# Optimization experiments

Measured on AMD Instinct MI355X. Metric: run time of the kernel, lower is better.

Reference implementation:

```python
import jax, jax.numpy as jnp
import numpy as np

EMB = 2048
HEADS = 16
HEAD_DIM = EMB // HEADS
MIN_WINDOW = 64
MAX_WINDOW = 256
ROPE_BASE = 10000.0


def setup_inputs() -> dict:
    key = jax.random.key(0)
    ks = jax.random.split(key, 5)
    B, S = 2, 2048
    x = jax.random.normal(ks[0], (B, S, EMB), dtype=jnp.float32)
    w_qkv = jax.random.normal(ks[1], (3 * EMB, EMB), dtype=jnp.float32) * (EMB ** -0.5)
    w_out = jax.random.normal(ks[2], (EMB, EMB), dtype=jnp.float32) * (EMB ** -0.5)
    w_c1 = jax.random.normal(ks[3], (EMB // 4, EMB), dtype=jnp.float32) * 0.1 * (EMB ** -0.5)
    w_c2 = jax.random.normal(ks[4], (1, EMB // 4), dtype=jnp.float32) * 0.1 * ((EMB // 4) ** -0.5)
    return {"x": x, "w_qkv": w_qkv, "w_out": w_out, "w_c1": w_c1, "w_c2": w_c2}


def _rotate_half(t):
    # interleaved pairs: [-x1, x0, -x3, x2, ...]
    x1 = t[..., ::2]
    x2 = t[..., 1::2]
    return jnp.stack((-x2, x1), axis=-1).reshape(t.shape)


def _rope_tables(seq_len, dtype):
    inv_freq = 1.0 / (ROPE_BASE ** (jnp.arange(0, HEAD_DIM, 2, dtype=jnp.float32) / HEAD_DIM))
    pos = jnp.arange(seq_len, dtype=jnp.float32)
    freqs = jnp.outer(pos, inv_freq)                      # [S, D/2]
    emb = jnp.concatenate([freqs, freqs], axis=-1)        # [S, D]
    return jnp.cos(emb)[None, None].astype(dtype), jnp.sin(emb)[None, None].astype(dtype)


def _forward(x, w_qkv, w_out, w_c1, w_c2):
    B, S, _ = x.shape
    scale = HEAD_DIM ** -0.5

    qkv = x @ w_qkv.T                                     # [B, S, 3E]
    qkv = qkv.reshape(B, S, 3, HEADS, HEAD_DIM).transpose(2, 0, 3, 1, 4)
    q, k, v = qkv[0], qkv[1], qkv[2]                      # each [B, H, S, D]

    cos, sin = _rope_tables(S, x.dtype)
    q = q * cos + _rotate_half(q) * sin
    k = k * cos + _rotate_half(k) * sin

    scores = jnp.einsum("bhqd,bhkd->bhqk", q, k) * scale  # [B, H, S, S]

    # adaptive window size from input complexity
    var = jnp.var(x.reshape(B, -1), axis=1, ddof=1)        # torch unbiased var over dims [1,2]
    var_norm = jax.nn.sigmoid(var * 10.0 - 5.0)
    x_mean = x.mean(axis=1)                                # [B, E]
    hidden = jax.nn.silu(x_mean @ w_c1.T)
    learned = jax.nn.sigmoid(hidden @ w_c2.T)[:, 0]        # [B]
    complexity = (var_norm + learned) / 2.0
    window_f = MIN_WINDOW + complexity * (MAX_WINDOW - MIN_WINDOW)
    window = window_f.mean().astype(jnp.int32)             # trunc like .int()
    window = jnp.maximum(jnp.minimum(window, S), MIN_WINDOW)

    # causal + sliding-window mask: keep 0 <= q_pos - k_pos < window
    pos = jnp.arange(S)
    rel = pos[:, None] - pos[None, :]                      # [S, S]
    keep = (rel >= 0) & (rel < window)
    scores = jnp.where(keep[None, None], scores, -jnp.inf)

    attn = jax.nn.softmax(scores, axis=-1)
    out = jnp.einsum("bhqk,bhkd->bhqd", attn, v)           # [B, H, S, D]
    out = out.transpose(0, 2, 1, 3).reshape(B, S, EMB)
    return out @ w_out.T


def reference(x, w_qkv, w_out, w_c1, w_c2):
    return _forward(x, w_qkv, w_out, w_c1, w_c2)
```

## Files before the change

### kernel.cpp

```cpp
#include <hip/hip_runtime.h>
#include <math.h>


#define S_LEN 2048
#define EMB 2048
#define HEADS 16
#define HDIM 128
#define NT 20
#define PSTR 336

typedef _Float16 f16x8 __attribute__((ext_vector_type(8)));
typedef _Float16 f16x4 __attribute__((ext_vector_type(4)));
typedef float f32x4 __attribute__((ext_vector_type(4)));

__device__ __forceinline__ void gld16(const void* g, void* l) {
    __builtin_amdgcn_global_load_lds(
        (const __attribute__((address_space(1))) unsigned int*)g,
        (__attribute__((address_space(3))) unsigned int*)l, 16, 0, 0);
}

__global__ void rope_table(float2* __restrict__ cstab) {
    int s = blockIdx.x;
    int d = threadIdx.x;
    int j = d & 63;
    double inv = pow(10000.0, -(double)j / 64.0);
    double ang = (double)s * inv;
    cstab[s * HDIM + d] = make_float2((float)cos(ang), (float)sin(ang));
}

__global__ __launch_bounds__(256) void col_reduce(const float* __restrict__ x,
                                                  float* __restrict__ xmean_acc,
                                                  double* __restrict__ scal,
                                                  _Float16* __restrict__ x16) {
    int b = blockIdx.z;
    int cg = blockIdx.x;
    int sg = blockIdx.y;
    int e4 = cg * 256 + threadIdx.x;
    const size_t base = ((size_t)b * S_LEN + sg * 32) * EMB;
    const float4* xb = (const float4*)(x + base) + e4;
    f16x4* xo = (f16x4*)(x16 + base) + e4;
    double cs0 = 0.0, cs1 = 0.0, cs2 = 0.0, cs3 = 0.0;
    double cq = 0.0;
    for (int s = 0; s < 32; ++s) {
        float4 v = xb[(size_t)s * (EMB / 4)];
        f16x4 o;
        o.x = (_Float16)v.x; o.y = (_Float16)v.y;
        o.z = (_Float16)v.z; o.w = (_Float16)v.w;
        xo[(size_t)s * (EMB / 4)] = o;
        cs0 += v.x; cs1 += v.y; cs2 += v.z; cs3 += v.w;
        cq += (double)v.x * v.x + (double)v.y * v.y +
              (double)v.z * v.z + (double)v.w * v.w;
    }
    float* xm = xmean_acc + b * EMB + e4 * 4;
    atomicAdd(xm + 0, (float)cs0);
    atomicAdd(xm + 1, (float)cs1);
    atomicAdd(xm + 2, (float)cs2);
    atomicAdd(xm + 3, (float)cs3);
    __shared__ double rs[256], rq[256];
    rs[threadIdx.x] = cs0 + cs1 + cs2 + cs3;
    rq[threadIdx.x] = cq;
    __syncthreads();
    for (int off = 128; off > 0; off >>= 1) {
        if (threadIdx.x < off) {
            rs[threadIdx.x] += rs[threadIdx.x + off];
            rq[threadIdx.x] += rq[threadIdx.x + off];
        }
        __syncthreads();
    }
    if (threadIdx.x == 0) {
        atomicAdd(&scal[b], rs[0]);
        atomicAdd(&scal[2 + b], rq[0]);
    }
}

__global__ __launch_bounds__(256) void hidden_kernel(const float* __restrict__ xmean_acc,
                                                     const float* __restrict__ wc1,
                                                     float* __restrict__ hidden) {
    int j = blockIdx.x;
    int b = blockIdx.y;
    const float* xm = xmean_acc + b * EMB;
    const float* wr = wc1 + (size_t)j * EMB;
    double acc = 0.0;
    for (int k = threadIdx.x; k < EMB; k += 256)
        acc += (double)xm[k] * (double)wr[k];
    __shared__ double red[256];
    red[threadIdx.x] = acc;
    __syncthreads();
    for (int off = 128; off > 0; off >>= 1) {
        if (threadIdx.x < off) red[threadIdx.x] += red[threadIdx.x + off];
        __syncthreads();
    }
    if (threadIdx.x == 0) {
        double z = red[0] * (1.0 / 2048.0);
        hidden[b * 512 + j] = (float)(z / (1.0 + exp(-z)));
    }
}

__global__ __launch_bounds__(512) void window_kernel(const float* __restrict__ hidden,
                                                     const float* __restrict__ wc2,
                                                     const double* __restrict__ scal,
                                                     int* __restrict__ wout) {
    __shared__ double red[512];
    __shared__ double wfs[2];
    for (int b = 0; b < 2; ++b) {
        red[threadIdx.x] = (double)hidden[b * 512 + threadIdx.x] * (double)wc2[threadIdx.x];
        __syncthreads();
        for (int off = 256; off > 0; off >>= 1) {
            if (threadIdx.x < off) red[threadIdx.x] += red[threadIdx.x + off];
            __syncthreads();
        }
        if (threadIdx.x == 0) {
            double pre = red[0];
            double learned = 1.0 / (1.0 + exp(-pre));
            const double N = (double)S_LEN * (double)EMB;
            double sum = scal[b], sq = scal[2 + b];
            double var = (sq - sum * sum / N) / (N - 1.0);
            double vn = 1.0 / (1.0 + exp(-(var * 10.0 - 5.0)));
            double comp = 0.5 * (vn + learned);
            wfs[b] = 64.0 + comp * 192.0;
        }
        __syncthreads();
    }
    if (threadIdx.x == 0) {
        float wf = (float)(0.5 * (wfs[0] + wfs[1]));
        int w = (int)wf;
        if (w > S_LEN) w = S_LEN;
        if (w < 64) w = 64;
        *wout = w;
    }
}

#define NQKV4 3145728
#define NOUT4 1048576
__global__ __launch_bounds__(256) void cvt_weights(const float* __restrict__ wqkv,
                                                   const float* __restrict__ wout,
                                                   _Float16* __restrict__ d_qkv,
                                                   _Float16* __restrict__ d_out) {
    int i = blockIdx.x * 256 + threadIdx.x;
    const float4* s;
    f16x4* d;
    if (i < NQKV4) {
        s = (const float4*)wqkv + i;
        d = (f16x4*)d_qkv + i;
    } else {
        s = (const float4*)wout + (i - NQKV4);
        d = (f16x4*)d_out + (i - NQKV4);
    }
    float4 v = *s;
    f16x4 o;
    o.x = (_Float16)v.x; o.y = (_Float16)v.y;
    o.z = (_Float16)v.z; o.w = (_Float16)v.w;
    *d = o;
}

#define GEMM_PROLOGUE(An, Wn)                                                   \
    __shared__ _Float16 As[128 * 64];                                           \
    __shared__ _Float16 Bs[128 * 64];                                           \
    const int tid = threadIdx.x;                                                \
    const int lane = tid & 63;                                                  \
    const int wv = tid >> 6;                                                    \
    const int wm = wv >> 1, wn = wv & 1;                                        \
    const int m0 = blockIdx.y * 128;                                            \
    const int n0 = blockIdx.x * 128;                                            \
    const int lrow = lane >> 3;                                       \
    const int lchk = (lane & 7) ^ lrow;                       \
    const int srow = wv * 32 + lrow;                                            \
    const _Float16* agp = An + (size_t)(m0 + srow) * EMB + lchk * 8;            \
    const _Float16* bgp = Wn + (size_t)(n0 + srow) * EMB + lchk * 8;            \
    _Float16* al = &As[wv * 32 * 64];                                           \
    _Float16* bl = &Bs[wv * 32 * 64];                                           \
    const int frow = lane & 15;                                                 \
    const int fgrp = lane >> 4;                                                 \
    f32x4 acc[4][4] = {};                                                       \
    for (int k0 = 0; k0 < EMB; k0 += 64) {                                      \
        __syncthreads();                                                        \
        _Pragma("unroll")                                                       \
        for (int t = 0; t < 4; ++t) {                                           \
            gld16(agp + (size_t)t * 8 * EMB, al + t * 8 * 64);                  \
            gld16(bgp + (size_t)t * 8 * EMB, bl + t * 8 * 64);                  \
        }                                                                       \
        agp += 64; bgp += 64;                                                   \
        __syncthreads();                                                        \
        _Pragma("unroll")                                                       \
        for (int ks = 0; ks < 2; ++ks) {                                        \
            f16x8 af[4], bf[4];                                                 \
            _Pragma("unroll")                                                   \
            for (int i = 0; i < 4; ++i)                                         \
                af[i] = *(const f16x8*)&As[(wm * 64 + i * 16 + frow) * 64 +     \
                                           (((ks * 4 + fgrp) ^ (frow & 7)) * 8)]; \
            _Pragma("unroll")                                                   \
            for (int j = 0; j < 4; ++j)                                         \
                bf[j] = *(const f16x8*)&Bs[(wn * 64 + j * 16 + frow) * 64 +     \
                                           (((ks * 4 + fgrp) ^ (frow & 7)) * 8)]; \
            _Pragma("unroll")                                                   \
            for (int i = 0; i < 4; ++i)                                         \
                _Pragma("unroll")                                               \
                for (int j = 0; j < 4; ++j)                                     \
                    acc[i][j] = __builtin_amdgcn_mfma_f32_16x16x32_f16(         \
                        af[i], bf[j], acc[i][j], 0, 0, 0);                      \
        }                                                                       \
    }                                                                           \
    const int colbase = lane & 15;                                              \
    const int rowoff = (lane >> 4) * 4;

__global__ __launch_bounds__(256) void gemm_qkv_f16(const _Float16* __restrict__ An,
                                                    const _Float16* __restrict__ Wn,
                                                    _Float16* __restrict__ q16,
                                                    _Float16* __restrict__ k16,
                                                    _Float16* __restrict__ vt,
                                                    const float2* __restrict__ cstab) {
    GEMM_PROLOGUE(An, Wn)
    const int which = n0 >> 11;
    const int h = (n0 >> 7) & 15;
    if (which == 2) {
#pragma unroll
        for (int i = 0; i < 4; ++i) {
#pragma unroll
            for (int j = 0; j < 4; ++j) {
                const int d = wn * 64 + j * 16 + colbase;
                int m = m0 + wm * 64 + i * 16 + rowoff;
                int b = m >> 11, s = m & 2047;
                f16x4 o;
#pragma unroll
                for (int r = 0; r < 4; ++r) o[r] = (_Float16)acc[i][j][r];
                *(f16x4*)&vt[(((size_t)b * HEADS + h) * HDIM + d) * S_LEN + s] = o;
            }
        }
    } else {
        _Float16* dst = which == 0 ? q16 : k16;
        const float sgn = (colbase & 1) ? 1.f : -1.f;
#pragma unroll
        for (int i = 0; i < 4; ++i) {
#pragma unroll
            for (int j = 0; j < 4; ++j) {
                const int d = wn * 64 + j * 16 + colbase;
#pragma unroll
                for (int r = 0; r < 4; ++r) {
                    int m = m0 + wm * 64 + i * 16 + rowoff + r;
                    int b = m >> 11, s = m & 2047;
                    float a = acc[i][j][r];
                    float p = __shfl_xor(a, 1, 64);
                    float2 cs = cstab[(size_t)s * HDIM + d];
                    float o = fmaf(a, cs.x, sgn * p * cs.y);
                    dst[(((size_t)b * HEADS + h) * S_LEN + s) * HDIM + d] = (_Float16)o;
                }
            }
        }
    }
}

__global__ __launch_bounds__(256) void gemm_out_f16(const _Float16* __restrict__ An,
                                                    const _Float16* __restrict__ Wn,
                                                    float* __restrict__ C) {
    GEMM_PROLOGUE(An, Wn)
#pragma unroll
    for (int i = 0; i < 4; ++i) {
#pragma unroll
        for (int j = 0; j < 4; ++j) {
            const int n = n0 + wn * 64 + j * 16 + colbase;
#pragma unroll
            for (int r = 0; r < 4; ++r) {
                int m = m0 + wm * 64 + i * 16 + rowoff + r;
                C[(size_t)m * EMB + n] = acc[i][j][r];
            }
        }
    }
}

__global__ __launch_bounds__(256) void attn_mfma(const _Float16* __restrict__ q16,
                                                 const _Float16* __restrict__ k16,
                                                 const _Float16* __restrict__ v16t,
                                                 _Float16* __restrict__ ob,
                                                 const int* __restrict__ wptr) {
    const int q0 = blockIdx.x * 64;
    const int h = blockIdx.y;
    const int b = blockIdx.z;
    const int tid = threadIdx.x;
    const int lane = tid & 63;
    const int wv = tid >> 6;
    const int w = *wptr;

    __shared__ _Float16 Pl[4][16 * PSTR];
    _Float16* Pw = Pl[wv];

    const int kstart = q0 - 256;
    int ntlo_w = ((257 - w) >> 4) + wv;
    int ntlo_n = q0 < 256 ? ((256 - q0) >> 4) : 0;
    const int lo = ntlo_w > ntlo_n ? ntlo_w : ntlo_n;
    const int hi = wv + 17;
    const int pvlo = lo >> 1;
    const int pvhi = (hi + 1) >> 1;
    const int plo2 = pvlo << 1;
    const int phi2 = pvhi << 1;

    const int frow = lane & 15;
    const int fgrp = lane >> 4;
    const int fcol = fgrp * 8;

    const size_t bh = (size_t)b * HEADS + h;
    const _Float16* Qp = q16 + (bh * S_LEN + q0 + wv * 16 + frow) * HDIM + fcol;
    const _Float16* Kb = k16 + bh * S_LEN * HDIM;
    const _Float16* Vt = v16t + bh * HDIM * S_LEN;

    f16x8 aq[4];
#pragma unroll
    for (int ks = 0; ks < 4; ++ks) aq[ks] = *(const f16x8*)(Qp + ks * 32);

    f32x4 accs[NT];
#pragma unroll
    for (int nt = 0; nt < NT; ++nt) accs[nt] = (f32x4){0.f, 0.f, 0.f, 0.f};
#pragma unroll
    for (int nt = 0; nt < NT; ++nt) {
        if (nt < lo || nt >= hi) continue;
        int krow = kstart + nt * 16 + frow;
        if (krow < 0) krow = 0;
        const _Float16* kp = Kb + (size_t)krow * HDIM + fcol;
#pragma unroll
        for (int ks = 0; ks < 4; ++ks) {
            f16x8 bk = *(const f16x8*)(kp + ks * 32);
            accs[nt] = __builtin_amdgcn_mfma_f32_16x16x32_f16(aq[ks], bk, accs[nt], 0, 0, 0);
        }
    }

    const int qrow = fgrp * 4;
    const int qabs = q0 + wv * 16 + qrow;
    const float scale = 0.08838834764831845f;
    float mx[4] = {-INFINITY, -INFINITY, -INFINITY, -INFINITY};
#pragma unroll
    for (int nt = 0; nt < NT; ++nt) {
        if (nt < lo || nt >= hi) continue;
        int key = kstart + nt * 16 + frow;
#pragma unroll
        for (int r = 0; r < 4; ++r) {
            int rel = (qabs + r) - key;
            bool keep = (key >= 0) && (rel >= 0) && (rel < w);
            float s = keep ? accs[nt][r] * scale : -INFINITY;
            accs[nt][r] = s;
            mx[r] = fmaxf(mx[r], s);
        }
    }
#pragma unroll
    for (int r = 0; r < 4; ++r) {
        float m = mx[r];
#pragma unroll
        for (int off = 1; off < 16; off <<= 1)
            m = fmaxf(m, __shfl_xor(m, off, 64));
        mx[r] = m;
    }

    float ls[4] = {0.f, 0.f, 0.f, 0.f};
#pragma unroll
    for (int nt = 0; nt < NT; ++nt) {
        if (nt < plo2 || nt >= phi2) continue;
        const bool alive = (nt >= lo) && (nt < hi);
#pragma unroll
        for (int r = 0; r < 4; ++r) {
            float p = alive ? __expf(accs[nt][r] - mx[r]) : 0.f;
            ls[r] += p;
            Pw[(qrow + r) * PSTR + nt * 16 + frow] = (_Float16)p;
        }
    }
    float inv[4];
#pragma unroll
    for (int r = 0; r < 4; ++r) {
        float l = ls[r];
#pragma unroll
        for (int off = 1; off < 16; off <<= 1)
            l += __shfl_xor(l, off, 64);
        inv[r] = 1.f / l;
    }

    f32x4 acco[8];
#pragma unroll
    for (int jt = 0; jt < 8; ++jt) acco[jt] = (f32x4){0.f, 0.f, 0.f, 0.f};
    const _Float16* Pr = &Pl[wv][frow * PSTR];
#pragma unroll
    for (int kp = 0; kp < 10; ++kp) {
        if (kp < pvlo || kp >= pvhi) continue;
        f16x8 ap = *(const f16x8*)(Pr + kp * 32 + fcol);
        int kv = kstart + kp * 32 + fcol;
        if (kv < 0) kv = 0;
#pragma unroll
        for (int jt = 0; jt < 8; ++jt) {
            f16x8 bv = *(const f16x8*)(Vt + (size_t)(jt * 16 + frow) * S_LEN + kv);
            acco[jt] = __builtin_amdgcn_mfma_f32_16x16x32_f16(ap, bv, acco[jt], 0, 0, 0);
        }
    }

#pragma unroll
    for (int jt = 0; jt < 8; ++jt) {
#pragma unroll
        for (int r = 0; r < 4; ++r) {
            int s = qabs + r;
            ob[((size_t)b * S_LEN + s) * EMB + h * HDIM + jt * 16 + frow] =
                (_Float16)(acco[jt][r] * inv[r]);
        }
    }
}

extern "C" void kernel_launch(void* const* d_in, const int* in_sizes, int n_in,
                              void* d_out, int out_size, void* d_ws, size_t ws_size,
                              hipStream_t stream) {
    const float* x     = (const float*)d_in[0];
    const float* w_qkv = (const float*)d_in[1];
    const float* w_out = (const float*)d_in[2];
    const float* w_c1  = (const float*)d_in[3];
    const float* w_c2  = (const float*)d_in[4];
    float* out = (float*)d_out;
    char* ws = (char*)d_ws;

    double*    scal   = (double*)(ws + 0);
    int*       win    = (int*)(ws + 64);
    float*     xmean  = (float*)(ws + 128);
    float*     hidden = (float*)(ws + 16640);
    float2*    cstab  = (float2*)(ws + 32768);
    _Float16*  x16    = (_Float16*)(ws + 4194304);
    _Float16*  wqkv16 = (_Float16*)(ws + 20971520);
    _Float16*  ao16   = (_Float16*)(ws + 20971520);
    _Float16*  v16t   = (_Float16*)(ws + 46137344);
    _Float16*  q16    = (_Float16*)(ws + 62914560);
    _Float16*  k16    = (_Float16*)(ws + 79691776);
    _Float16*  wout16 = (_Float16*)(ws + 96468992);

    hipMemsetAsync(d_ws, 0, 32768, stream);

    rope_table<<<dim3(S_LEN), dim3(HDIM), 0, stream>>>(cstab);
    col_reduce<<<dim3(2, 64, 2), dim3(256), 0, stream>>>(x, xmean, scal, x16);
    hidden_kernel<<<dim3(512, 2), dim3(256), 0, stream>>>(xmean, w_c1, hidden);
    window_kernel<<<dim3(1), dim3(512), 0, stream>>>(hidden, w_c2, scal, win);

    cvt_weights<<<dim3((NQKV4 + NOUT4) / 256), dim3(256), 0, stream>>>(
        w_qkv, w_out, wqkv16, wout16);

    gemm_qkv_f16<<<dim3(48, 32), dim3(256), 0, stream>>>(x16, wqkv16, q16, k16, v16t, cstab);
    attn_mfma<<<dim3(32, HEADS, 2), dim3(256), 0, stream>>>(q16, k16, v16t, ao16, win);
    gemm_out_f16<<<dim3(16, 32), dim3(256), 0, stream>>>(ao16, wout16, out);
}
```

Baseline: 397.3 us.

## Rewrite QKV GEMM as 256x256-tile, 8-wave, multi-buffered pipelined kernel

Replaces the 128x128, 4-wave QKV projection GEMM with a 256x256 tile computed by 8 waves. Global loads go directly to LDS and are multi-buffered, with explicit vmcnt waits, barriers, sched_barrier and setprio so that MFMA work overlaps with the loads. It also remaps block indices into a grouped order to improve L2 reuse. The larger tile raises data reuse per load but cuts the grid to 384 blocks, which risks low occupancy and wave-quantization on a 256-CU device. The hand-tuned wait counts must match the load issue order exactly.

```diff
diff --git a/kernel.cpp b/kernel.cpp
--- a/kernel.cpp
+++ b/kernel.cpp
@@ -151,6 +151,171 @@
     o.x = (_Float16)v.x; o.y = (_Float16)v.y;
     o.z = (_Float16)v.z; o.w = (_Float16)v.w;
     *d = o;
+}
+
+
+#define STG_A(bufc, ksc, kofs)                                              \
+    gld16(aSrc + (kofs), &Ap[bufc][ksc][wv * 512]);                         \
+    gld16(aSrc + (kofs) + (size_t)128 * EMB, &Ap[bufc][ksc][4096 + wv * 512]);
+#define STG_B(bufc, ksc, kofs)                                              \
+    gld16(bSrc + (kofs), &Bp[bufc][ksc][wv * 512]);                         \
+    gld16(bSrc + (kofs) + (size_t)128 * EMB, &Bp[bufc][ksc][4096 + wv * 512]);
+
+#define VM8 asm volatile("s_waitcnt vmcnt(8)" ::: "memory");
+#define VM4 asm volatile("s_waitcnt vmcnt(4)" ::: "memory");
+#define VM0 asm volatile("s_waitcnt vmcnt(0)" ::: "memory");
+#define VMN
+
+#define QPH_A(bufc, ksc, VM, ...)                                           \
+    {                                                                       \
+        f16x8 af[4];                                                        \
+        _Pragma("unroll")                                                   \
+        for (int j_ = 0; j_ < 4; ++j_)                                      \
+            bf[j_] = *(const f16x8*)&Bp[bufc][ksc][boff0 + j_ * 512];       \
+        _Pragma("unroll")                                                   \
+        for (int i_ = 0; i_ < 4; ++i_)                                      \
+            af[i_] = *(const f16x8*)&Ap[bufc][ksc][aoff0 + i_ * 512];       \
+        __VA_ARGS__                                                         \
+        __builtin_amdgcn_sched_barrier(0);                                  \
+        __builtin_amdgcn_s_barrier();                                       \
+        asm volatile("s_waitcnt lgkmcnt(0)" ::: "memory");                  \
+        __builtin_amdgcn_sched_barrier(0);                                  \
+        __builtin_amdgcn_s_setprio(1);                                      \
+        _Pragma("unroll")                                                   \
+        for (int i_ = 0; i_ < 4; ++i_)                                      \
+            _Pragma("unroll")                                               \
+            for (int j_ = 0; j_ < 4; ++j_)                                  \
+                acc[i_][j_] = __builtin_amdgcn_mfma_f32_16x16x32_f16(       \
+                    af[i_], bf[j_], acc[i_][j_], 0, 0, 0);                  \
+        __builtin_amdgcn_s_setprio(0);                                      \
+        __builtin_amdgcn_sched_barrier(0);                                  \
+        VM                                                                  \
+        __builtin_amdgcn_s_barrier();                                       \
+        __builtin_amdgcn_sched_barrier(0);                                  \
+    }
+
+#define QPH_B(bufc, ksc, VM, ...)                                           \
+    {                                                                       \
+        f16x8 af[4];                                                        \
+        _Pragma("unroll")                                                   \
+        for (int i_ = 0; i_ < 4; ++i_)                                      \
+            af[i_] = *(const f16x8*)&Ap[bufc][ksc][aoff0 + 2048 + i_ * 512];\
+        __VA_ARGS__                                                         \
+        __builtin_amdgcn_sched_barrier(0);                                  \
+        __builtin_amdgcn_s_barrier();                                       \
+        asm volatile("s_waitcnt lgkmcnt(0)" ::: "memory");                  \
+        __builtin_amdgcn_sched_barrier(0);                                  \
+        __builtin_amdgcn_s_setprio(1);                                      \
+        _Pragma("unroll")                                                   \
+        for (int i_ = 0; i_ < 4; ++i_)                                      \
+            _Pragma("unroll")                                               \
+            for (int j_ = 0; j_ < 4; ++j_)                                  \
+                acc[4 + i_][j_] = __builtin_amdgcn_mfma_f32_16x16x32_f16(   \
+                    af[i_], bf[j_], acc[4 + i_][j_], 0, 0, 0);              \
+        __builtin_amdgcn_s_setprio(0);                                      \
+        __builtin_amdgcn_sched_barrier(0);                                  \
+        VM                                                                  \
+        __builtin_amdgcn_s_barrier();                                       \
+        __builtin_amdgcn_sched_barrier(0);                                  \
+    }
+
+__global__ __launch_bounds__(512, 2) void gemm_qkv_f16(const _Float16* __restrict__ An,
+                                                       const _Float16* __restrict__ Wn,
+                                                       _Float16* __restrict__ q16,
+                                                       _Float16* __restrict__ k16,
+                                                       _Float16* __restrict__ vt,
+                                                       const float2* __restrict__ cstab) {
+    __shared__ __align__(16) _Float16 Ap[2][2][8192];
+    __shared__ __align__(16) _Float16 Bp[2][2][8192];
+    const int tid = threadIdx.x;
+    const int lane = tid & 63;
+    const int wv = tid >> 6;
+    const int wm = wv >> 2;
+    const int wn = wv & 3;
+    const int f = blockIdx.y * 24 + blockIdx.x;
+    const int fs = (f & 7) * 48 + (f >> 3);
+    const int m0 = (fs / 24) * 256;
+    const int n0 = (fs % 24) * 256;
+    const int srow = tid >> 2;
+    const int schk = tid & 3;
+    const _Float16* aSrc = An + (size_t)(m0 + srow) * EMB + schk * 8;
+    const _Float16* bSrc = Wn + (size_t)(n0 + srow) * EMB + schk * 8;
+    const int frow = lane & 15;
+    const int fgrp = lane >> 4;
+    const int aoff0 = (wm * 128 + frow) * 32 + fgrp * 8;
+    const int boff0 = (wn * 64 + frow) * 32 + fgrp * 8;
+    f32x4 acc[8][4] = {};
+    f16x8 bf[4];
+
+    STG_A(0, 0, 0) STG_B(0, 0, 0)
+    STG_A(0, 1, 32) STG_B(0, 1, 32)
+    STG_A(1, 0, 64) STG_B(1, 0, 64)
+    VM8
+    __builtin_amdgcn_s_barrier();
+    __builtin_amdgcn_sched_barrier(0);
+
+    for (int it = 0; it < 15; ++it) {
+        QPH_A(0, 0, VMN, STG_A(1, 1, 96))
+        QPH_B(0, 0, VM8, STG_B(1, 1, 96))
+        QPH_A(0, 1, VMN, STG_A(0, 0, 128))
+        QPH_B(0, 1, VM8, STG_B(0, 0, 128))
+        QPH_A(1, 0, VMN, STG_A(0, 1, 160))
+        QPH_B(1, 0, VM8, STG_B(0, 1, 160))
+        QPH_A(1, 1, VMN, STG_A(1, 0, 192))
+        QPH_B(1, 1, VM8, STG_B(1, 0, 192))
+        aSrc += 128;
+        bSrc += 128;
+    }
+    QPH_A(0, 0, VMN, STG_A(1, 1, 96))
+    QPH_B(0, 0, VM8, STG_B(1, 1, 96))
+    QPH_A(0, 1, VMN)
+    QPH_B(0, 1, VM4)
+    QPH_A(1, 0, VMN)
+    QPH_B(1, 0, VM0)
+    QPH_A(1, 1, VMN)
+    QPH_B(1, 1, VMN)
+
+    const int colbase = lane & 15;
+    const int rowoff = fgrp * 4;
+    const int nb = n0 + wn * 64;
+    const int which = nb >> 11;
+    const int h = (nb >> 7) & 15;
+    const int d0 = nb & 127;
+    if (which == 2) {
+#pragma unroll
+        for (int i = 0; i < 8; ++i) {
+#pragma unroll
+            for (int j = 0; j < 4; ++j) {
+                const int d = d0 + j * 16 + colbase;
+                int m = m0 + wm * 128 + i * 16 + rowoff;
+                int b = m >> 11, s = m & 2047;
+                f16x4 o;
+#pragma unroll
+                for (int r = 0; r < 4; ++r) o[r] = (_Float16)acc[i][j][r];
+                *(f16x4*)&vt[(((size_t)b * HEADS + h) * HDIM + d) * S_LEN + s] = o;
+            }
+        }
+    } else {
+        _Float16* dst = which == 0 ? q16 : k16;
+        const float sgn = (colbase & 1) ? 1.f : -1.f;
+#pragma unroll
+        for (int i = 0; i < 8; ++i) {
+#pragma unroll
+            for (int j = 0; j < 4; ++j) {
+                const int d = d0 + j * 16 + colbase;
+#pragma unroll
+                for (int r = 0; r < 4; ++r) {
+                    int m = m0 + wm * 128 + i * 16 + rowoff + r;
+                    int b = m >> 11, s = m & 2047;
+                    float a = acc[i][j][r];
+                    float p = __shfl_xor(a, 1, 64);
+                    float2 cs = cstab[(size_t)s * HDIM + d];
+                    float o = fmaf(a, cs.x, sgn * p * cs.y);
+                    dst[(((size_t)b * HEADS + h) * S_LEN + s) * HDIM + d] = (_Float16)o;
+                }
+            }
+        }
+    }
 }
 
 #define GEMM_PROLOGUE(An, Wn)                                                   \
@@ -203,52 +368,6 @@
     const int colbase = lane & 15;                                              \
     const int rowoff = (lane >> 4) * 4;
 
-__global__ __launch_bounds__(256) void gemm_qkv_f16(const _Float16* __restrict__ An,
-                                                    const _Float16* __restrict__ Wn,
-                                                    _Float16* __restrict__ q16,
-                                                    _Float16* __restrict__ k16,
-                                                    _Float16* __restrict__ vt,
-                                                    const float2* __restrict__ cstab) {
-    GEMM_PROLOGUE(An, Wn)
-    const int which = n0 >> 11;
-    const int h = (n0 >> 7) & 15;
-    if (which == 2) {
-#pragma unroll
-        for (int i = 0; i < 4; ++i) {
-#pragma unroll
-            for (int j = 0; j < 4; ++j) {
-                const int d = wn * 64 + j * 16 + colbase;
-                int m = m0 + wm * 64 + i * 16 + rowoff;
-                int b = m >> 11, s = m & 2047;
-                f16x4 o;
-#pragma unroll
-                for (int r = 0; r < 4; ++r) o[r] = (_Float16)acc[i][j][r];
-                *(f16x4*)&vt[(((size_t)b * HEADS + h) * HDIM + d) * S_LEN + s] = o;
-            }
-        }
-    } else {
-        _Float16* dst = which == 0 ? q16 : k16;
-        const float sgn = (colbase & 1) ? 1.f : -1.f;
-#pragma unroll
-        for (int i = 0; i < 4; ++i) {
-#pragma unroll
-            for (int j = 0; j < 4; ++j) {
-                const int d = wn * 64 + j * 16 + colbase;
-#pragma unroll
-                for (int r = 0; r < 4; ++r) {
-                    int m = m0 + wm * 64 + i * 16 + rowoff + r;
-                    int b = m >> 11, s = m & 2047;
-                    float a = acc[i][j][r];
-                    float p = __shfl_xor(a, 1, 64);
-                    float2 cs = cstab[(size_t)s * HDIM + d];
-                    float o = fmaf(a, cs.x, sgn * p * cs.y);
-                    dst[(((size_t)b * HEADS + h) * S_LEN + s) * HDIM + d] = (_Float16)o;
-                }
-            }
-        }
-    }
-}
-
 __global__ __launch_bounds__(256) void gemm_out_f16(const _Float16* __restrict__ An,
                                                     const _Float16* __restrict__ Wn,
                                                     float* __restrict__ C) {
@@ -432,7 +551,7 @@
     cvt_weights<<<dim3((NQKV4 + NOUT4) / 256), dim3(256), 0, stream>>>(
         w_qkv, w_out, wqkv16, wout16);
 
-    gemm_qkv_f16<<<dim3(48, 32), dim3(256), 0, stream>>>(x16, wqkv16, q16, k16, v16t, cstab);
+    gemm_qkv_f16<<<dim3(24, 16), dim3(512), 0, stream>>>(x16, wqkv16, q16, k16, v16t, cstab);
     attn_mfma<<<dim3(32, HEADS, 2), dim3(256), 0, stream>>>(q16, k16, v16t, ao16, win);
     gemm_out_f16<<<dim3(16, 32), dim3(256), 0, stream>>>(ao16, wout16, out);
 }
```

New measurement: 411.1 us. 3.5% more time.

## Rewrite QKV GEMM as 256x256 tile with double-buffered LDS pipeline

Applied to the files above, without the earlier changes.

Replaces the 128x128 QKV projection GEMM with a 512-thread, 256x256-tile kernel. It stages tiles with global_load_lds into double-buffered LDS halves, using explicit vmcnt waits, barriers, sched_barriers and setprio around MFMA bursts so loads overlap compute. The RoPE table kernel also moves from double-precision pow/cos/sin to float exp2f/cosf/sinf. The intent is to raise data reuse and hide memory latency in the largest GEMM, at the cost of more registers and LDS per block, fewer blocks, and slightly less accurate RoPE angles at large positions.

```diff
diff --git a/kernel.cpp b/kernel.cpp
--- a/kernel.cpp
+++ b/kernel.cpp
@@ -23,9 +23,9 @@
     int s = blockIdx.x;
     int d = threadIdx.x;
     int j = d & 63;
-    double inv = pow(10000.0, -(double)j / 64.0);
-    double ang = (double)s * inv;
-    cstab[s * HDIM + d] = make_float2((float)cos(ang), (float)sin(ang));
+    float inv = exp2f(-13.287712379549449f * (float)j * (1.0f / 64.0f));
+    float ang = (float)s * inv;
+    cstab[s * HDIM + d] = make_float2(cosf(ang), sinf(ang));
 }
 
 __global__ __launch_bounds__(256) void col_reduce(const float* __restrict__ x,
@@ -151,6 +151,136 @@
     o.x = (_Float16)v.x; o.y = (_Float16)v.y;
     o.z = (_Float16)v.z; o.w = (_Float16)v.w;
     *d = o;
+}
+
+
+#define STG(bufc, hc, kofs)                                                 \
+    gld16(aS0 + (kofs), &Ap[bufc][hc][wv * 512]);                           \
+    gld16(aS1 + (kofs), &Ap[bufc][hc][4096 + wv * 512]);                    \
+    gld16(bS0 + (kofs), &Bp[bufc][hc][wv * 512]);                           \
+    gld16(bS1 + (kofs), &Bp[bufc][hc][4096 + wv * 512]);
+
+#define VM8 asm volatile("s_waitcnt vmcnt(8)" ::: "memory");
+#define VM4 asm volatile("s_waitcnt vmcnt(4)" ::: "memory");
+#define VM0 asm volatile("s_waitcnt vmcnt(0)" ::: "memory");
+#define VMN
+
+#define PH(bufc, hc, VM, ...)                                               \
+    {                                                                       \
+        f16x8 af[8], bf[4];                                                 \
+        _Pragma("unroll")                                                   \
+        for (int j_ = 0; j_ < 4; ++j_)                                      \
+            bf[j_] = *(const f16x8*)&Bp[bufc][hc][bbase + j_ * 512];        \
+        _Pragma("unroll")                                                   \
+        for (int i_ = 0; i_ < 8; ++i_)                                      \
+            af[i_] = *(const f16x8*)&Ap[bufc][hc][abase + i_ * 512];        \
+        __VA_ARGS__                                                         \
+        __builtin_amdgcn_sched_barrier(0);                                  \
+        __builtin_amdgcn_s_barrier();                                       \
+        asm volatile("s_waitcnt lgkmcnt(0)" ::: "memory");                  \
+        __builtin_amdgcn_sched_barrier(0);                                  \
+        __builtin_amdgcn_s_setprio(1);                                      \
+        _Pragma("unroll")                                                   \
+        for (int i_ = 0; i_ < 8; ++i_)                                      \
+            _Pragma("unroll")                                               \
+            for (int j_ = 0; j_ < 4; ++j_)                                  \
+                acc[i_][j_] = __builtin_amdgcn_mfma_f32_16x16x32_f16(       \
+                    af[i_], bf[j_], acc[i_][j_], 0, 0, 0);                  \
+        __builtin_amdgcn_s_setprio(0);                                      \
+        __builtin_amdgcn_sched_barrier(0);                                  \
+        VM                                                                  \
+        __builtin_amdgcn_s_barrier();                                       \
+        __builtin_amdgcn_sched_barrier(0);                                  \
+    }
+
+__global__ __launch_bounds__(512, 2) void gemm_qkv_f16(const _Float16* __restrict__ An,
+                                                       const _Float16* __restrict__ Wn,
+                                                       _Float16* __restrict__ q16,
+                                                       _Float16* __restrict__ k16,
+                                                       _Float16* __restrict__ vt,
+                                                       const float2* __restrict__ cstab) {
+    __shared__ __align__(16) _Float16 Ap[2][2][8192];
+    __shared__ __align__(16) _Float16 Bp[2][2][8192];
+    const int tid = threadIdx.x;
+    const int lane = tid & 63;
+    const int wv = tid >> 6;
+    const int wm = wv >> 2;
+    const int wn = wv & 3;
+    const int m0 = blockIdx.y * 256;
+    const int n0 = blockIdx.x * 256;
+    const int g = (lane & 7) ^ (lane >> 3);
+    const int rb = 2 * (lane >> 3) + (g >> 2);
+    const int kq = (g & 3) * 8;
+    const _Float16* aS0 = An + (size_t)(m0 + wv * 16 + rb) * EMB + kq;
+    const _Float16* aS1 = aS0 + (size_t)128 * EMB;
+    const _Float16* bS0 = Wn + (size_t)(n0 + wv * 16 + rb) * EMB + kq;
+    const _Float16* bS1 = bS0 + (size_t)128 * EMB;
+    const int frow = lane & 15;
+    const int fgrp = lane >> 4;
+    const int srl = frow >> 1;
+    const int cst = ((((frow & 1) << 2) + fgrp) ^ srl);
+    const int abase = (wm * 64 + srl) * 64 + cst * 8;
+    const int bbase = (wn * 32 + srl) * 64 + cst * 8;
+    f32x4 acc[8][4] = {};
+
+    STG(0, 0, 0) STG(0, 1, 32) STG(1, 0, 64) STG(1, 1, 96)
+    VM8
+    __builtin_amdgcn_s_barrier();
+    __builtin_amdgcn_sched_barrier(0);
+
+    PH(0, 0, VM8)
+    PH(0, 1, VM4)
+    for (int it = 0; it < 15; ++it) {
+        PH(1, 0, VM8, STG(0, 0, 128) STG(0, 1, 160))
+        PH(1, 1, VM4)
+        PH(0, 0, VM8, STG(1, 0, 192) STG(1, 1, 224))
+        PH(0, 1, VM4)
+        aS0 += 128; aS1 += 128; bS0 += 128; bS1 += 128;
+    }
+    PH(1, 0, VM0)
+    PH(1, 1, VMN)
+
+    const int colbase = lane & 15;
+    const int rowoff = fgrp * 4;
+    const int nb = n0 + wn * 64;
+    const int which = nb >> 11;
+    const int h = (nb >> 7) & 15;
+    const int d0 = nb & 127;
+    if (which == 2) {
+#pragma unroll
+        for (int i = 0; i < 8; ++i) {
+#pragma unroll
+            for (int j = 0; j < 4; ++j) {
+                const int d = d0 + j * 16 + colbase;
+                int m = m0 + wm * 128 + i * 16 + rowoff;
+                int b = m >> 11, s = m & 2047;
+                f16x4 o;
+#pragma unroll
+                for (int r = 0; r < 4; ++r) o[r] = (_Float16)acc[i][j][r];
+                *(f16x4*)&vt[(((size_t)b * HEADS + h) * HDIM + d) * S_LEN + s] = o;
+            }
+        }
+    } else {
+        _Float16* dst = which == 0 ? q16 : k16;
+        const float sgn = (colbase & 1) ? 1.f : -1.f;
+#pragma unroll
+        for (int i = 0; i < 8; ++i) {
+#pragma unroll
+            for (int j = 0; j < 4; ++j) {
+                const int d = d0 + j * 16 + colbase;
+#pragma unroll
+                for (int r = 0; r < 4; ++r) {
+                    int m = m0 + wm * 128 + i * 16 + rowoff + r;
+                    int b = m >> 11, s = m & 2047;
+                    float a = acc[i][j][r];
+                    float p = __shfl_xor(a, 1, 64);
+                    float2 cs = cstab[(size_t)s * HDIM + d];
+                    float o = fmaf(a, cs.x, sgn * p * cs.y);
+                    dst[(((size_t)b * HEADS + h) * S_LEN + s) * HDIM + d] = (_Float16)o;
+                }
+            }
+        }
+    }
 }
 
 #define GEMM_PROLOGUE(An, Wn)                                                   \
@@ -203,52 +333,6 @@
     const int colbase = lane & 15;                                              \
     const int rowoff = (lane >> 4) * 4;
 
-__global__ __launch_bounds__(256) void gemm_qkv_f16(const _Float16* __restrict__ An,
-                                                    const _Float16* __restrict__ Wn,
-                                                    _Float16* __restrict__ q16,
-                                                    _Float16* __restrict__ k16,
-                                                    _Float16* __restrict__ vt,
-                                                    const float2* __restrict__ cstab) {
-    GEMM_PROLOGUE(An, Wn)
-    const int which = n0 >> 11;
-    const int h = (n0 >> 7) & 15;
-    if (which == 2) {
-#pragma unroll
-        for (int i = 0; i < 4; ++i) {
-#pragma unroll
-            for (int j = 0; j < 4; ++j) {
-                const int d = wn * 64 + j * 16 + colbase;
-                int m = m0 + wm * 64 + i * 16 + rowoff;
-                int b = m >> 11, s = m & 2047;
-                f16x4 o;
-#pragma unroll
-                for (int r = 0; r < 4; ++r) o[r] = (_Float16)acc[i][j][r];
-                *(f16x4*)&vt[(((size_t)b * HEADS + h) * HDIM + d) * S_LEN + s] = o;
-            }
-        }
-    } else {
-        _Float16* dst = which == 0 ? q16 : k16;
-        const float sgn = (colbase & 1) ? 1.f : -1.f;
-#pragma unroll
-        for (int i = 0; i < 4; ++i) {
-#pragma unroll
-            for (int j = 0; j < 4; ++j) {
-                const int d = wn * 64 + j * 16 + colbase;
-#pragma unroll
-                for (int r = 0; r < 4; ++r) {
-                    int m = m0 + wm * 64 + i * 16 + rowoff + r;
-                    int b = m >> 11, s = m & 2047;
-                    float a = acc[i][j][r];
-                    float p = __shfl_xor(a, 1, 64);
-                    float2 cs = cstab[(size_t)s * HDIM + d];
-                    float o = fmaf(a, cs.x, sgn * p * cs.y);
-                    dst[(((size_t)b * HEADS + h) * S_LEN + s) * HDIM + d] = (_Float16)o;
-                }
-            }
-        }
-    }
-}
-
 __global__ __launch_bounds__(256) void gemm_out_f16(const _Float16* __restrict__ An,
                                                     const _Float16* __restrict__ Wn,
                                                     float* __restrict__ C) {
@@ -432,7 +516,7 @@
     cvt_weights<<<dim3((NQKV4 + NOUT4) / 256), dim3(256), 0, stream>>>(
         w_qkv, w_out, wqkv16, wout16);
 
-    gemm_qkv_f16<<<dim3(48, 32), dim3(256), 0, stream>>>(x16, wqkv16, q16, k16, v16t, cstab);
+    gemm_qkv_f16<<<dim3(24, 16), dim3(512), 0, stream>>>(x16, wqkv16, q16, k16, v16t, cstab);
     attn_mfma<<<dim3(32, HEADS, 2), dim3(256), 0, stream>>>(q16, k16, v16t, ao16, win);
     gemm_out_f16<<<dim3(16, 32), dim3(256), 0, stream>>>(ao16, wout16, out);
 }
```

New measurement: 423.2 us. +6.5%, slower.
